# Kernel tuning notes

Measured on AMD Instinct MI355X. Metric: run time of the kernel, lower is better.

Reference implementation:

```python
import jax, jax.numpy as jnp
import numpy as np

EMB = 512
HEAD = 8
HEAD_DIM = EMB // HEAD


def setup_inputs() -> dict:
    key = jax.random.key(0)
    ks = jax.random.split(key, 12)
    B, S = 2, 4096
    scale = 1.0 / np.sqrt(EMB)
    inp = {
        "q": jax.random.normal(ks[0], (B, S, EMB), dtype=jnp.float32),
        "kv": jax.random.normal(ks[1], (B, S, EMB), dtype=jnp.float32),
        "Wq": jax.random.normal(ks[2], (EMB, EMB), dtype=jnp.float32) * scale,
        "bq": jax.random.normal(ks[3], (EMB,), dtype=jnp.float32) * 0.01,
        "Wk": jax.random.normal(ks[4], (EMB, EMB), dtype=jnp.float32) * scale,
        "bk": jax.random.normal(ks[5], (EMB,), dtype=jnp.float32) * 0.01,
        "Wv": jax.random.normal(ks[6], (EMB, EMB), dtype=jnp.float32) * scale,
        "bv": jax.random.normal(ks[7], (EMB,), dtype=jnp.float32) * 0.01,
        "Wo": jax.random.normal(ks[8], (EMB, EMB), dtype=jnp.float32) * scale,
        "bo": jax.random.normal(ks[9], (EMB,), dtype=jnp.float32) * 0.01,
    }
    return inp


def reference(q, kv, Wq, bq, Wk, bk, Wv, bv, Wo, bo):
    B, N, _ = q.shape
    M = kv.shape[1]
    # Linear projections (torch Linear: x @ W^T + b)
    qh = (q @ Wq.T + bq).reshape(B, N, HEAD, HEAD_DIM).transpose(0, 2, 1, 3)  # [B,H,N,d]
    kh = (kv @ Wk.T + bk).reshape(B, M, HEAD, HEAD_DIM).transpose(0, 2, 1, 3)  # [B,H,M,d]
    vh = (kv @ Wv.T + bv).reshape(B, M, HEAD, HEAD_DIM).transpose(0, 2, 1, 3)  # [B,H,M,d]
    attn = jnp.einsum("bhnd,bhmd->bhnm", qh, kh) / jnp.sqrt(jnp.float32(HEAD_DIM))
    attn = jax.nn.softmax(attn, axis=-1)
    out = jnp.einsum("bhnm,bhmd->bhnd", attn, vh)  # [B,H,N,d]
    out = out.transpose(0, 2, 1, 3).reshape(B, N, EMB)
    out = out @ Wo.T + bo
    return out
```

## Files before the change

kernel.cpp:

```cpp
#include <hip/hip_runtime.h>
#include <stdint.h>

typedef unsigned short u16;
typedef __attribute__((ext_vector_type(8))) short short8;
typedef __attribute__((ext_vector_type(4))) float f32x4;
typedef __attribute__((ext_vector_type(16))) float f32x16;

typedef __attribute__((address_space(1))) void as1_void;
typedef __attribute__((address_space(3))) void as3_void;

__device__ inline u16 f2bf(float x) {
  uint32_t u = __float_as_uint(x);
  return (u16)((u + 0x7fffu + ((u >> 16) & 1u)) >> 16);
}

__device__ inline void gload16(const void* g, void* l) {
  __builtin_amdgcn_global_load_lds((as1_void*)g, (as3_void*)l, 16, 0, 0);
}

__device__ inline uint32_t cvtpk(float lo, float hi) {
  uint32_t d;
  asm("v_cvt_pk_bf16_f32 %0, %1, %2" : "=v"(d) : "v"(lo), "v"(hi));
  return d;
}

__device__ inline void plswap(uint32_t& a, uint32_t& b) {
  asm("v_permlane32_swap_b32 %0, %1" : "+v"(a), "+v"(b));
}

__device__ inline float fexp2(float x) {
  float r;
  asm("v_exp_f32 %0, %1" : "=v"(r) : "v"(x));
  return r;
}

__global__ __launch_bounds__(256) void cvt_all(const float* __restrict__ q,
                                               const float* __restrict__ kv,
                                               const float* __restrict__ Wq,
                                               const float* __restrict__ Wk,
                                               const float* __restrict__ Wv,
                                               const float* __restrict__ Wo,
                                               u16* __restrict__ qb,
                                               u16* __restrict__ kvb,
                                               u16* __restrict__ wall) {
  const int bx = blockIdx.x;
  const float* in;
  u16* out;
  int i;
  if (bx < 4096) {
    in = q; out = qb; i = bx * 256 + threadIdx.x;
  } else if (bx < 8192) {
    in = kv; out = kvb; i = (bx - 4096) * 256 + threadIdx.x;
  } else {
    int widx = (bx - 8192) >> 8;
    in = (widx == 0) ? Wq : (widx == 1) ? Wk : (widx == 2) ? Wv : Wo;
    out = wall + (size_t)widx * 262144;
    i = ((bx - 8192) & 255) * 256 + threadIdx.x;
  }
  float4 v = ((const float4*)in)[i];
  ushort4 o;
  o.x = f2bf(v.x); o.y = f2bf(v.y); o.z = f2bf(v.z); o.w = f2bf(v.w);
  ((ushort4*)out)[i] = o;
}

__global__ __launch_bounds__(256) void gemm_qkv(const u16* __restrict__ qb,
                                                const u16* __restrict__ kvb,
                                                const u16* __restrict__ wq,
                                                const u16* __restrict__ wk,
                                                const u16* __restrict__ wv,
                                                const float* __restrict__ bq,
                                                const float* __restrict__ bk,
                                                const float* __restrict__ bv,
                                                u16* __restrict__ Qh,
                                                u16* __restrict__ Kh,
                                                u16* __restrict__ Vt, float qscale) {
  __shared__ __align__(16) char smem[49152];
  const int z = blockIdx.z;
  const u16* A = (z == 0) ? qb : kvb;
  const u16* W = (z == 0) ? wq : (z == 1) ? wk : wv;
  const float* bias = (z == 0) ? bq : (z == 1) ? bk : bv;
  const float prescale = (z == 0) ? qscale : 1.0f;
  u16* Cout = (z == 0) ? Qh : (z == 1) ? Kh : Vt;

  const int tid = threadIdx.x;
  const int lane = tid & 63;
  const int wv_ = tid >> 6;
  const int c = lane & 15;
  const int g = lane >> 4;
  const int wr = wv_ >> 1, wc = wv_ & 1;
  const int m0 = blockIdx.x * 64;
  const int n0 = blockIdx.y * 128;

  const int r0 = tid >> 3, cc = tid & 7;
  const int u0 = cc ^ (r0 & 7);
  const u16* srcA0 = A + (size_t)(m0 + r0) * 512 + u0 * 8;
  const u16* srcW0 = W + (size_t)(n0 + r0) * 512 + u0 * 8;

#define GEMM_STAGE(BUF, KK)                              \
  {                                                      \
    char* ab_ = (char*)smem + (BUF)*24576 + wv_ * 1024;  \
    gload16(srcA0 + (KK), ab_);                          \
    gload16(srcA0 + (KK) + 16384, ab_ + 4096);           \
    gload16(srcW0 + (KK), ab_ + 8192);                   \
    gload16(srcW0 + (KK) + 16384, ab_ + 12288);          \
    gload16(srcW0 + (KK) + 32768, ab_ + 16384);          \
    gload16(srcW0 + (KK) + 49152, ab_ + 20480);          \
  }

  f32x4 acc[2][4];
#pragma unroll
  for (int i = 0; i < 2; i++)
#pragma unroll
    for (int j = 0; j < 4; j++) acc[i][j] = (f32x4){0.f, 0.f, 0.f, 0.f};

  GEMM_STAGE(0, 0)
  __syncthreads();
  int cur = 0;
  const int swa = c & 7;
  for (int it = 0; it < 8; ++it) {
    if (it < 7) GEMM_STAGE(cur ^ 1, (it + 1) * 64)
    const u16* Ab = (const u16*)((char*)smem + cur * 24576);
    const u16* Wb = Ab + 4096;
#pragma unroll
    for (int kd = 0; kd < 2; kd++) {
      short8 af[2], wf[4];
#pragma unroll
      for (int ai = 0; ai < 2; ai++)
        af[ai] = *(const short8*)&Ab[(wr * 32 + ai * 16 + c) * 64 + (((kd * 4 + g) ^ swa) << 3)];
#pragma unroll
      for (int bj = 0; bj < 4; bj++)
        wf[bj] = *(const short8*)&Wb[(wc * 64 + bj * 16 + c) * 64 + (((kd * 4 + g) ^ swa) << 3)];
#pragma unroll
      for (int ai = 0; ai < 2; ai++)
#pragma unroll
        for (int bj = 0; bj < 4; bj++)
          acc[ai][bj] = __builtin_amdgcn_mfma_f32_16x16x32_bf16(af[ai], wf[bj], acc[ai][bj], 0, 0, 0);
    }
    __syncthreads();
    cur ^= 1;
  }

#pragma unroll
  for (int ai = 0; ai < 2; ai++)
#pragma unroll
    for (int bj = 0; bj < 4; bj++)
#pragma unroll
      for (int r = 0; r < 4; r++) {
        int m = m0 + wr * 32 + ai * 16 + g * 4 + r;
        int n = n0 + wc * 64 + bj * 16 + c;
        float v = (acc[ai][bj][r] + bias[n]) * prescale;
        int b = m >> 12, s = m & 4095;
        int h = n >> 6, d = n & 63;
        size_t idx;
        if (z < 2)
          idx = ((size_t)(b * 8 + h) * 4096 + s) * 64 + d;
        else
          idx = ((size_t)(b * 8 + h) * 64 + d) * 4096 + s;
        Cout[idx] = f2bf(v);
      }
}

__global__ __launch_bounds__(256) void gemm_out(const u16* __restrict__ A,
                                                const u16* __restrict__ W,
                                                const float* __restrict__ bias,
                                                float* __restrict__ Cout) {
  __shared__ __align__(16) char smem[49152];
  const int tid = threadIdx.x;
  const int lane = tid & 63;
  const int wv_ = tid >> 6;
  const int c = lane & 15;
  const int g = lane >> 4;
  const int wr = wv_ >> 1, wc = wv_ & 1;
  const int m0 = blockIdx.x * 64;
  const int n0 = blockIdx.y * 128;

  const int r0 = tid >> 3, cc = tid & 7;
  const int u0 = cc ^ (r0 & 7);
  const u16* srcA0 = A + (size_t)(m0 + r0) * 512 + u0 * 8;
  const u16* srcW0 = W + (size_t)(n0 + r0) * 512 + u0 * 8;

  f32x4 acc[2][4];
#pragma unroll
  for (int i = 0; i < 2; i++)
#pragma unroll
    for (int j = 0; j < 4; j++) acc[i][j] = (f32x4){0.f, 0.f, 0.f, 0.f};

  GEMM_STAGE(0, 0)
  __syncthreads();
  int cur = 0;
  const int swa = c & 7;
  for (int it = 0; it < 8; ++it) {
    if (it < 7) GEMM_STAGE(cur ^ 1, (it + 1) * 64)
    const u16* Ab = (const u16*)((char*)smem + cur * 24576);
    const u16* Wb = Ab + 4096;
#pragma unroll
    for (int kd = 0; kd < 2; kd++) {
      short8 af[2], wf[4];
#pragma unroll
      for (int ai = 0; ai < 2; ai++)
        af[ai] = *(const short8*)&Ab[(wr * 32 + ai * 16 + c) * 64 + (((kd * 4 + g) ^ swa) << 3)];
#pragma unroll
      for (int bj = 0; bj < 4; bj++)
        wf[bj] = *(const short8*)&Wb[(wc * 64 + bj * 16 + c) * 64 + (((kd * 4 + g) ^ swa) << 3)];
#pragma unroll
      for (int ai = 0; ai < 2; ai++)
#pragma unroll
        for (int bj = 0; bj < 4; bj++)
          acc[ai][bj] = __builtin_amdgcn_mfma_f32_16x16x32_bf16(af[ai], wf[bj], acc[ai][bj], 0, 0, 0);
    }
    __syncthreads();
    cur ^= 1;
  }

#pragma unroll
  for (int ai = 0; ai < 2; ai++)
#pragma unroll
    for (int bj = 0; bj < 4; bj++)
#pragma unroll
      for (int r = 0; r < 4; r++) {
        int m = m0 + wr * 32 + ai * 16 + g * 4 + r;
        int n = n0 + wc * 64 + bj * 16 + c;
        Cout[(size_t)m * 512 + n] = acc[ai][bj][r] + bias[n];
      }
}

__global__ __launch_bounds__(256) void attn_split(const u16* __restrict__ Qh,
                                                  const u16* __restrict__ Kh,
                                                  const u16* __restrict__ Vt,
                                                  float* __restrict__ Op,
                                                  float* __restrict__ Ml) {
  __shared__ __align__(16) char smem[32768];
  const int tid = threadIdx.x;
  const int lane = tid & 63;
  const int w = tid >> 6;
  const int c5 = lane & 31;
  const int h = lane >> 5;
  const int bid = (blockIdx.x & 7) * 128 + (blockIdx.x >> 3);
  const int half = bid & 1;
  const int qt = (bid >> 1) & 31;
  const int bh = bid >> 6;
  const int q0 = qt * 128 + w * 32;
  const u16* Qb = Qh + (size_t)bh * 262144;
  const u16* Kb = Kh + (size_t)bh * 262144 + (size_t)half * 2048 * 64;
  const u16* Vb = Vt + (size_t)bh * 262144 + half * 2048;

  short8 qf[4];
#pragma unroll
  for (int kd = 0; kd < 4; kd++)
    qf[kd] = *(const short8*)(Qb + (size_t)(q0 + c5) * 64 + kd * 16 + h * 8);

  f32x16 accO[2];
#pragma unroll
  for (int i = 0; i < 16; i++) { accO[0][i] = 0.f; accO[1][i] = 0.f; }
  float l_r = 0.f;

  const int r = tid >> 4, p = tid & 15;
  const int x = p ^ r;
  const int gb = x >> 3, ge = x & 7;
  const u16* srcKA = Kb + (size_t)(r + 32 * gb) * 64 + ge * 8;
  const u16* srcKB = Kb + (size_t)(16 + r + 32 * gb) * 64 + ge * 8;
  const u16* srcVA = Vb + (size_t)(r + 32 * gb) * 4096 + ge * 8;
  const u16* srcVB = Vb + (size_t)(16 + r + 32 * gb) * 4096 + ge * 8;

#define ATTN_STAGE(BUF, T)                                \
  {                                                       \
    char* b_ = (char*)smem + (BUF)*16384 + w * 1024;      \
    gload16(srcKA + (size_t)(T)*4096, b_);                \
    gload16(srcKB + (size_t)(T)*4096, b_ + 4096);         \
    gload16(srcVA + (T)*64, b_ + 8192);                   \
    gload16(srcVB + (T)*64, b_ + 12288);                  \
  }

  ATTN_STAGE(0, 0)
  __syncthreads();
  const int swz = c5 & 15;
  const int rowb = c5 * 128;

  short8 pa_prev[4];
  short8 vf_prev[8];

  for (int t = 0; t < 32; ++t) {
    const int cur = t & 1;
    if (t < 31) ATTN_STAGE(cur ^ 1, t + 1)

    const u16* Kl = (const u16*)(smem + cur * 16384);
    const u16* Vl = Kl + 4096;

    f32x16 s0, s1;
#pragma unroll
    for (int i = 0; i < 16; i++) { s0[i] = 0.f; s1[i] = 0.f; }
    __builtin_amdgcn_s_setprio(1);
#pragma unroll
    for (int kd = 0; kd < 4; kd++) {
      short8 kf0 = *(const short8*)&Kl[rowb + ((((kd << 1) + h) ^ swz) << 3)];
      short8 kf1 = *(const short8*)&Kl[rowb + (((8 + (kd << 1) + h) ^ swz) << 3)];
      s0 = __builtin_amdgcn_mfma_f32_32x32x16_bf16(kf0, qf[kd], s0, 0, 0, 0);
      s1 = __builtin_amdgcn_mfma_f32_32x32x16_bf16(kf1, qf[kd], s1, 0, 0, 0);
    }
    if (t > 0) {
#pragma unroll
      for (int km = 0; km < 4; km++) {
        accO[0] = __builtin_amdgcn_mfma_f32_32x32x16_bf16(vf_prev[2 * km], pa_prev[km], accO[0], 0, 0, 0);
        accO[1] = __builtin_amdgcn_mfma_f32_32x32x16_bf16(vf_prev[2 * km + 1], pa_prev[km], accO[1], 0, 0, 0);
      }
    }
    __builtin_amdgcn_s_setprio(0);
    __builtin_amdgcn_sched_barrier(0);

#pragma unroll
    for (int i = 0; i < 16; i++) { s0[i] = fexp2(s0[i]); s1[i] = fexp2(s1[i]); }

    float tsum0 = ((s0[0] + s1[0]) + (s0[4] + s1[4])) + ((s0[8] + s1[8]) + (s0[12] + s1[12]));
    float tsum1 = ((s0[1] + s1[1]) + (s0[5] + s1[5])) + ((s0[9] + s1[9]) + (s0[13] + s1[13]));
    float tsum2 = ((s0[2] + s1[2]) + (s0[6] + s1[6])) + ((s0[10] + s1[10]) + (s0[14] + s1[14]));
    float tsum3 = ((s0[3] + s1[3]) + (s0[7] + s1[7])) + ((s0[11] + s1[11]) + (s0[15] + s1[15]));
    float rsq = (tsum0 + tsum1) + (tsum2 + tsum3);
    l_r += rsq + __shfl_xor(rsq, 32);

    uint32_t pk0[4][2], pk1[4][2];
#pragma unroll
    for (int u = 0; u < 4; u++) {
      pk0[u][0] = cvtpk(s0[4 * u], s0[4 * u + 1]);
      pk0[u][1] = cvtpk(s0[4 * u + 2], s0[4 * u + 3]);
      pk1[u][0] = cvtpk(s1[4 * u], s1[4 * u + 1]);
      pk1[u][1] = cvtpk(s1[4 * u + 2], s1[4 * u + 3]);
    }
#pragma unroll
    for (int km = 0; km < 2; km++) {
      const int uA = (km & 1) * 2, uB = uA + 1;
      uint32_t a0 = pk0[uA][0], b0 = pk0[uB][0]; plswap(a0, b0);
      uint32_t a1 = pk0[uA][1], b1 = pk0[uB][1]; plswap(a1, b1);
      union { uint32_t u[4]; short8 s; } uu;
      uu.u[0] = a0; uu.u[1] = a1; uu.u[2] = b0; uu.u[3] = b1;
      pa_prev[km] = uu.s;
    }
#pragma unroll
    for (int km = 2; km < 4; km++) {
      const int uA = (km & 1) * 2, uB = uA + 1;
      uint32_t a0 = pk1[uA][0], b0 = pk1[uB][0]; plswap(a0, b0);
      uint32_t a1 = pk1[uA][1], b1 = pk1[uB][1]; plswap(a1, b1);
      union { uint32_t u[4]; short8 s; } uu;
      uu.u[0] = a0; uu.u[1] = a1; uu.u[2] = b0; uu.u[3] = b1;
      pa_prev[km] = uu.s;
    }

#pragma unroll
    for (int km = 0; km < 4; km++) {
      vf_prev[2 * km]     = *(const short8*)&Vl[rowb + ((((km << 1) + h) ^ swz) << 3)];
      vf_prev[2 * km + 1] = *(const short8*)&Vl[rowb + (((8 + (km << 1) + h) ^ swz) << 3)];
    }

    __syncthreads();
  }

#pragma unroll
  for (int km = 0; km < 4; km++) {
    accO[0] = __builtin_amdgcn_mfma_f32_32x32x16_bf16(vf_prev[2 * km], pa_prev[km], accO[0], 0, 0, 0);
    accO[1] = __builtin_amdgcn_mfma_f32_32x32x16_bf16(vf_prev[2 * km + 1], pa_prev[km], accO[1], 0, 0, 0);
  }

  const size_t pbase = (size_t)(half * 16 + bh) * 4096 + q0 + c5;
  float* Opw = Op + pbase * 64;
#pragma unroll
  for (int db = 0; db < 2; db++)
#pragma unroll
    for (int rr = 0; rr < 16; rr++) {
      int d = db * 32 + 4 * h + (rr & 3) + 8 * (rr >> 2);
      Opw[d] = accO[db][rr];
    }
  if (h == 0) { Ml[pbase * 2] = 0.f; Ml[pbase * 2 + 1] = l_r; }
}

__global__ __launch_bounds__(256) void attn_combine(const float* __restrict__ Op,
                                                    const float* __restrict__ Ml,
                                                    u16* __restrict__ aO) {
  int tg = blockIdx.x * 256 + threadIdx.x;
  int bhq = tg >> 3, seg = tg & 7;
  const float* p0 = Op + (size_t)bhq * 64 + seg * 8;
  const float* p1 = p0 + 4194304;
  float m0 = Ml[bhq * 2], l0 = Ml[bhq * 2 + 1];
  float m1 = Ml[131072 + bhq * 2], l1 = Ml[131072 + bhq * 2 + 1];
  float ms = fmaxf(m0, m1);
  float a0 = fexp2(m0 - ms), a1 = fexp2(m1 - ms);
  float inv = 1.f / (l0 * a0 + l1 * a1);
  float4 x0 = ((const float4*)p0)[0], x1 = ((const float4*)p0)[1];
  float4 y0 = ((const float4*)p1)[0], y1 = ((const float4*)p1)[1];
  ushort4 o0, o1;
  o0.x = f2bf((x0.x * a0 + y0.x * a1) * inv);
  o0.y = f2bf((x0.y * a0 + y0.y * a1) * inv);
  o0.z = f2bf((x0.z * a0 + y0.z * a1) * inv);
  o0.w = f2bf((x0.w * a0 + y0.w * a1) * inv);
  o1.x = f2bf((x1.x * a0 + y1.x * a1) * inv);
  o1.y = f2bf((x1.y * a0 + y1.y * a1) * inv);
  o1.z = f2bf((x1.z * a0 + y1.z * a1) * inv);
  o1.w = f2bf((x1.w * a0 + y1.w * a1) * inv);
  int bh = bhq >> 12, q = bhq & 4095;
  int b = bh >> 3, hh = bh & 7;
  u16* dst = aO + ((size_t)(b * 4096 + q)) * 512 + hh * 64 + seg * 8;
  ((ushort4*)dst)[0] = o0;
  ((ushort4*)dst)[1] = o1;
}

extern "C" void kernel_launch(void* const* d_in, const int* in_sizes, int n_in,
                              void* d_out, int out_size, void* d_ws, size_t ws_size,
                              hipStream_t stream) {
  const float* q  = (const float*)d_in[0];
  const float* kv = (const float*)d_in[1];
  const float* Wq = (const float*)d_in[2];
  const float* bq = (const float*)d_in[3];
  const float* Wk = (const float*)d_in[4];
  const float* bk = (const float*)d_in[5];
  const float* Wv = (const float*)d_in[6];
  const float* bv = (const float*)d_in[7];
  const float* Wo = (const float*)d_in[8];
  const float* bo = (const float*)d_in[9];

  const size_t MB = 1u << 20;
  char* ws = (char*)d_ws;
  u16* qb  = (u16*)(ws + 0 * MB);
  u16* kvb = (u16*)(ws + 8 * MB);
  u16* wqb = (u16*)(ws + 16 * MB);
  u16* wkb = (u16*)(ws + 16 * MB + 524288);
  u16* wvb = (u16*)(ws + 17 * MB);
  u16* wob = (u16*)(ws + 17 * MB + 524288);
  u16* Qh  = (u16*)(ws + 18 * MB);
  u16* Kh  = (u16*)(ws + 26 * MB);
  u16* Vt  = (u16*)(ws + 34 * MB);
  u16* aO  = (u16*)(ws + 42 * MB);
  float* Op = (float*)(ws + 50 * MB);
  float* Ml = (float*)(ws + 84 * MB);

  cvt_all<<<dim3(9216), dim3(256), 0, stream>>>(q, kv, Wq, Wk, Wv, Wo, qb, kvb, wqb);

  const float qscale = 0.125f * 1.44269504088896340736f;
  gemm_qkv<<<dim3(128, 4, 3), dim3(256), 0, stream>>>(qb, kvb, wqb, wkb, wvb,
                                                      bq, bk, bv, Qh, Kh, Vt, qscale);

  attn_split<<<dim3(1024), dim3(256), 0, stream>>>(Qh, Kh, Vt, Op, Ml);
  attn_combine<<<dim3(2048), dim3(256), 0, stream>>>(Op, Ml, aO);

  gemm_out<<<dim3(128, 4), dim3(256), 0, stream>>>(aO, wob, bo, (float*)d_out);
}
```

Before: 140.0 us.

## Fuse split-KV combine into attention kernel via last-arriver atomic counter

Removes the separate attn_combine launch. Each split-KV block writes its partial output and row sum with agent-scope stores, then bumps a per-tile counter. The second block to finish reads its partner's partial, normalizes, and writes the bf16 attention output through shared memory with coalesced stores. This saves a kernel launch and half of the partial-output round trip, at the cost of fences, atomics, and a serialized tail in the last-arriving block. The counters are zeroed by an extra block in the conversion kernel.

Measured after the change: 297.6 us. 113% more time.

```diff
diff --git a/kernel.cpp b/kernel.cpp
--- a/kernel.cpp
+++ b/kernel.cpp
@@ -32,6 +32,13 @@
   float r;
   asm("v_exp_f32 %0, %1" : "=v"(r) : "v"(x));
   return r;
+}
+
+__device__ inline void coh_store(float* p, float v) {
+  __hip_atomic_store(p, v, __ATOMIC_RELAXED, __HIP_MEMORY_SCOPE_AGENT);
+}
+__device__ inline float coh_load(const float* p) {
+  return __hip_atomic_load(p, __ATOMIC_RELAXED, __HIP_MEMORY_SCOPE_AGENT);
 }
 
 __global__ __launch_bounds__(256) void cvt_all(const float* __restrict__ q,
@@ -42,8 +49,14 @@
                                                const float* __restrict__ Wo,
                                                u16* __restrict__ qb,
                                                u16* __restrict__ kvb,
-                                               u16* __restrict__ wall) {
+                                               u16* __restrict__ wall,
+                                               int* __restrict__ cnt) {
   const int bx = blockIdx.x;
+  if (bx >= 9216) {
+    cnt[threadIdx.x] = 0;
+    cnt[256 + threadIdx.x] = 0;
+    return;
+  }
   const float* in;
   u16* out;
   int i;
@@ -228,8 +241,11 @@
                                                   const u16* __restrict__ Kh,
                                                   const u16* __restrict__ Vt,
                                                   float* __restrict__ Op,
-                                                  float* __restrict__ Ml) {
+                                                  float* __restrict__ Lw,
+                                                  int* __restrict__ cnt,
+                                                  u16* __restrict__ aO) {
   __shared__ __align__(16) char smem[32768];
+  __shared__ int oldv;
   const int tid = threadIdx.x;
   const int lane = tid & 63;
   const int w = tid >> 6;
@@ -366,39 +382,39 @@
 #pragma unroll
     for (int rr = 0; rr < 16; rr++) {
       int d = db * 32 + 4 * h + (rr & 3) + 8 * (rr >> 2);
-      Opw[d] = accO[db][rr];
-    }
-  if (h == 0) { Ml[pbase * 2] = 0.f; Ml[pbase * 2 + 1] = l_r; }
-}
-
-__global__ __launch_bounds__(256) void attn_combine(const float* __restrict__ Op,
-                                                    const float* __restrict__ Ml,
-                                                    u16* __restrict__ aO) {
-  int tg = blockIdx.x * 256 + threadIdx.x;
-  int bhq = tg >> 3, seg = tg & 7;
-  const float* p0 = Op + (size_t)bhq * 64 + seg * 8;
-  const float* p1 = p0 + 4194304;
-  float m0 = Ml[bhq * 2], l0 = Ml[bhq * 2 + 1];
-  float m1 = Ml[131072 + bhq * 2], l1 = Ml[131072 + bhq * 2 + 1];
-  float ms = fmaxf(m0, m1);
-  float a0 = fexp2(m0 - ms), a1 = fexp2(m1 - ms);
-  float inv = 1.f / (l0 * a0 + l1 * a1);
-  float4 x0 = ((const float4*)p0)[0], x1 = ((const float4*)p0)[1];
-  float4 y0 = ((const float4*)p1)[0], y1 = ((const float4*)p1)[1];
-  ushort4 o0, o1;
-  o0.x = f2bf((x0.x * a0 + y0.x * a1) * inv);
-  o0.y = f2bf((x0.y * a0 + y0.y * a1) * inv);
-  o0.z = f2bf((x0.z * a0 + y0.z * a1) * inv);
-  o0.w = f2bf((x0.w * a0 + y0.w * a1) * inv);
-  o1.x = f2bf((x1.x * a0 + y1.x * a1) * inv);
-  o1.y = f2bf((x1.y * a0 + y1.y * a1) * inv);
-  o1.z = f2bf((x1.z * a0 + y1.z * a1) * inv);
-  o1.w = f2bf((x1.w * a0 + y1.w * a1) * inv);
-  int bh = bhq >> 12, q = bhq & 4095;
-  int b = bh >> 3, hh = bh & 7;
-  u16* dst = aO + ((size_t)(b * 4096 + q)) * 512 + hh * 64 + seg * 8;
-  ((ushort4*)dst)[0] = o0;
-  ((ushort4*)dst)[1] = o1;
+      coh_store(&Opw[d], accO[db][rr]);
+    }
+  if (h == 0) coh_store(&Lw[pbase], l_r);
+
+  __threadfence();
+  __syncthreads();
+  if (tid == 0) oldv = atomicAdd(&cnt[(bh << 5) + qt], 1);
+  __syncthreads();
+  if (oldv != 1) return;
+  __threadfence();
+
+  const size_t obase = (size_t)((half ^ 1) * 16 + bh) * 4096 + q0 + c5;
+  const float* Os = Op + obase * 64;
+  const float inv = 1.f / (l_r + coh_load(&Lw[obase]));
+  u16* tile = (u16*)smem;
+#pragma unroll
+  for (int db = 0; db < 2; db++)
+#pragma unroll
+    for (int rr = 0; rr < 16; rr++) {
+      int d = db * 32 + 4 * h + (rr & 3) + 8 * (rr >> 2);
+      tile[(w * 32 + c5) * 64 + d] = f2bf((accO[db][rr] + coh_load(&Os[d])) * inv);
+    }
+  __syncthreads();
+  {
+    const int row = tid >> 1, hf = tid & 1;
+    const int b = bh >> 3, hh = bh & 7;
+    u16* dst = aO + ((size_t)(b * 4096 + qt * 128 + row)) * 512 + hh * 64 + hf * 32;
+    const u16* src = tile + row * 64 + hf * 32;
+    ((int4*)dst)[0] = ((const int4*)src)[0];
+    ((int4*)dst)[1] = ((const int4*)src)[1];
+    ((int4*)dst)[2] = ((const int4*)src)[2];
+    ((int4*)dst)[3] = ((const int4*)src)[3];
+  }
 }
 
 extern "C" void kernel_launch(void* const* d_in, const int* in_sizes, int n_in,
@@ -428,16 +444,16 @@
   u16* Vt  = (u16*)(ws + 34 * MB);
   u16* aO  = (u16*)(ws + 42 * MB);
   float* Op = (float*)(ws + 50 * MB);
-  float* Ml = (float*)(ws + 84 * MB);
-
-  cvt_all<<<dim3(9216), dim3(256), 0, stream>>>(q, kv, Wq, Wk, Wv, Wo, qb, kvb, wqb);
+  float* Lw = (float*)(ws + 84 * MB);
+  int*   cnt = (int*)(ws + 85 * MB);
+
+  cvt_all<<<dim3(9217), dim3(256), 0, stream>>>(q, kv, Wq, Wk, Wv, Wo, qb, kvb, wqb, cnt);
 
   const float qscale = 0.125f * 1.44269504088896340736f;
   gemm_qkv<<<dim3(128, 4, 3), dim3(256), 0, stream>>>(qb, kvb, wqb, wkb, wvb,
                                                       bq, bk, bv, Qh, Kh, Vt, qscale);
 
-  attn_split<<<dim3(1024), dim3(256), 0, stream>>>(Qh, Kh, Vt, Op, Ml);
-  attn_combine<<<dim3(2048), dim3(256), 0, stream>>>(Op, Ml, aO);
+  attn_split<<<dim3(1024), dim3(256), 0, stream>>>(Qh, Kh, Vt, Op, Lw, cnt, aO);
 
   gemm_out<<<dim3(128, 4), dim3(256), 0, stream>>>(aO, wob, bo, (float*)d_out);
 }
```
